# Kernel optimization log

Hardware: AMD Instinct MI355X
Metric: run time of the kernel (lower is better)

## Reference

```python
import jax, jax.numpy as jnp
import numpy as np

N = 50000      # nodes
E = 1600000    # edges (avg degree 32)
D_IN = 128
H = 256        # 2 * out_channels
D_OUT = 128
NEG_SLOPE = 0.2


def setup_inputs() -> dict:
    key = jax.random.key(0)
    ks = jax.random.split(key, 16)
    x = jax.random.normal(ks[0], (N, D_IN), dtype=jnp.float32)
    edge_index = jax.random.randint(ks[1], (2, E), 0, N, dtype=jnp.int64)

    def lin(k, fan_in, fan_out):
        s = 1.0 / np.sqrt(fan_in)
        return jax.random.uniform(k, (fan_in, fan_out), jnp.float32, -s, s)

    def att(k, d):
        s = 1.0 / np.sqrt(d)
        return jax.random.uniform(k, (d,), jnp.float32, -s, s)

    return {
        "x": x, "edge_index": edge_index,
        "W1": lin(ks[2], D_IN, H), "a1_src": att(ks[3], H), "a1_dst": att(ks[4], H), "b1": jnp.zeros((H,), jnp.float32),
        "W2": lin(ks[5], H, H),    "a2_src": att(ks[6], H), "a2_dst": att(ks[7], H), "b2": jnp.zeros((H,), jnp.float32),
        "W3": lin(ks[8], H, D_OUT),"a3_src": att(ks[9], D_OUT), "a3_dst": att(ks[10], D_OUT), "b3": jnp.zeros((D_OUT,), jnp.float32),
    }


def _gat_conv(x, W, a_src, a_dst, b, src, dst):
    # x: [N, Cin] -> h: [N, Cout]
    h = x @ W
    # per-node attention logits, gathered along edges (edge j->i: src=j, dst=i)
    e = jax.nn.leaky_relu((h @ a_src)[src] + (h @ a_dst)[dst], NEG_SLOPE)  # [E]
    # segment softmax over incoming edges of each destination node
    m = jax.ops.segment_max(e, dst, num_segments=N)          # [N]
    p = jnp.exp(e - m[dst])                                  # [E]
    denom = jax.ops.segment_sum(p, dst, num_segments=N)      # [N]
    alpha = p / denom[dst]                                   # [E]
    # scatter-add weighted source features
    out = jax.ops.segment_sum(alpha[:, None] * h[src], dst, num_segments=N)
    return out + b


def reference(x, edge_index, W1, a1_src, a1_dst, b1, W2, a2_src, a2_dst, b2, W3, a3_src, a3_dst, b3):
    src, dst = edge_index[0], edge_index[1]
    h = jax.nn.relu(_gat_conv(x, W1, a1_src, a1_dst, b1, src, dst))
    for _ in range(2):  # hidden_layers, shared conv2 weights
        h = jax.nn.relu(_gat_conv(h, W2, a2_src, a2_dst, b2, src, dst))
    out = _gat_conv(h, W3, a3_src, a3_dst, b3, src, dst)
    return jax.nn.softmax(out, axis=1)
```

## Files before the change

### kernel.cpp

```cpp
#include <hip/hip_runtime.h>
#include <hip/hip_bf16.h>
#include <hip/hip_fp16.h>

#define NN 50000
#define EE 1600000
#define DIN 128
#define HH 256
#define DOUT 128

typedef __attribute__((ext_vector_type(8))) short short8;
typedef __attribute__((ext_vector_type(4))) float f32x4;

__device__ __forceinline__ short f2bf(float v) {
    union { float f; unsigned u; } a;
    a.f = v;
    unsigned r = a.u + 0x7fffu + ((a.u >> 16) & 1u);
    return (short)(r >> 16);
}
__device__ __forceinline__ float bf2f(short h) {
    union { unsigned u; float f; } a;
    a.u = ((unsigned)(unsigned short)h) << 16;
    return a.f;
}


__global__ __launch_bounds__(256) void hist_kernel(const int* __restrict__ dst, int* __restrict__ deg, int E) {
    int e = blockIdx.x * 256 + threadIdx.x;
    if (e < E) atomicAdd(&deg[dst[e]], 1);
}

#define SCAN_B 256

__global__ __launch_bounds__(SCAN_B) void scan1_kernel(const int* __restrict__ deg, int* __restrict__ exc,
                                                       int* __restrict__ bsum, int n) {
    __shared__ int tmp[SCAN_B];
    int i = blockIdx.x * SCAN_B + threadIdx.x;
    int v = (i < n) ? deg[i] : 0;
    tmp[threadIdx.x] = v;
    __syncthreads();
    for (int o = 1; o < SCAN_B; o <<= 1) {
        int t = (threadIdx.x >= o) ? tmp[threadIdx.x - o] : 0;
        __syncthreads();
        tmp[threadIdx.x] += t;
        __syncthreads();
    }
    if (i < n) exc[i] = tmp[threadIdx.x] - v;
    if (threadIdx.x == SCAN_B - 1) bsum[blockIdx.x] = tmp[SCAN_B - 1];
}

__global__ __launch_bounds__(SCAN_B) void scan2_kernel(int* __restrict__ bsum, int nb) {
    __shared__ int tmp[SCAN_B];
    int v = (threadIdx.x < nb) ? bsum[threadIdx.x] : 0;
    tmp[threadIdx.x] = v;
    __syncthreads();
    for (int o = 1; o < SCAN_B; o <<= 1) {
        int t = (threadIdx.x >= o) ? tmp[threadIdx.x - o] : 0;
        __syncthreads();
        tmp[threadIdx.x] += t;
        __syncthreads();
    }
    if (threadIdx.x < nb) bsum[threadIdx.x] = tmp[threadIdx.x] - v;
}

__global__ __launch_bounds__(SCAN_B) void scan3_kernel(int* __restrict__ exc, const int* __restrict__ bsum,
                                                       int* __restrict__ cursor, int n, int E) {
    int i = blockIdx.x * SCAN_B + threadIdx.x;
    if (i < n) {
        int v = exc[i] + bsum[blockIdx.x];
        exc[i] = v;
        cursor[i] = v;
    }
    if (i == n) exc[n] = E;
}

#define NCB 256

__global__ __launch_bounds__(256) void scatter8_kernel(const int* __restrict__ src, const int* __restrict__ dst,
                                                       int* __restrict__ cursor, int* __restrict__ es, int E, int n) {
    int q = blockIdx.x & 7;
    int cb = blockIdx.x >> 3;
    int lo = q * (n >> 3);
    int hi = (q == 7) ? n : lo + (n >> 3);
    int chunk = (E + NCB - 1) / NCB;
    int e1 = min((cb + 1) * chunk, E);
    for (int e = cb * chunk + threadIdx.x; e < e1; e += 256) {
        int d = dst[e];
        if (d >= lo && d < hi) {
            int pos = atomicAdd(&cursor[d], 1);
            es[pos] = src[e];
        }
    }
}


__global__ __launch_bounds__(256) void wsplit_kernel(const float* __restrict__ W, short* __restrict__ WhT,
                                                     short* __restrict__ WlT, int K, int C) {
    int f = blockIdx.x * 256 + threadIdx.x;
    if (f >= K * C) return;
    int k = f / C, c = f % C;
    float v = W[f];
    short h = f2bf(v);
    short l = f2bf(v - bf2f(h));
    WhT[(size_t)c * K + k] = h;
    WlT[(size_t)c * K + k] = l;
}


__global__ __launch_bounds__(256) void tohalf_kernel(const float* __restrict__ in, __half* __restrict__ out,
                                                     size_t cnt) {
    size_t i = (size_t)(blockIdx.x * 256 + threadIdx.x) * 4;
    if (i + 3 < cnt) {
        float4 v = *(const float4*)(in + i);
        __half h0 = __float2half(v.x), h1 = __float2half(v.y);
        __half h2 = __float2half(v.z), h3 = __float2half(v.w);
        __half2* op = (__half2*)(out + i);
        op[0] = __half2(h0, h1);
        op[1] = __half2(h2, h3);
    }
}


template <bool BRELU, bool DOTS, bool HOUT, bool AHIN>
__global__ __launch_bounds__(256) void gemm_mfma_kernel(const float* __restrict__ X, const short* __restrict__ BhT,
                                                        const short* __restrict__ BlT, const float* __restrict__ bias,
                                                        float* __restrict__ out, const float* __restrict__ a1v,
                                                        const float* __restrict__ a2v, float* __restrict__ s1,
                                                        float* __restrict__ s2, int n, int K, int Cout) {
    __shared__ short Ah[128][40], Al[128][40];
    __shared__ short Bh[128][40], Bl[128][40];
    int tid = threadIdx.x;
    int row0 = blockIdx.y * 128, col0 = blockIdx.x * 128;
    int lane = tid & 63, wid = tid >> 6;
    int wr = (wid >> 1) * 64, wc = (wid & 1) * 64;

    f32x4 acc[4][4];
#pragma unroll
    for (int mi = 0; mi < 4; ++mi)
#pragma unroll
        for (int ni = 0; ni < 4; ++ni) acc[mi][ni] = 0.f;

    int srow = tid >> 1;
    int sk = (tid & 1) * 16;

    for (int k0 = 0; k0 < K; k0 += 32) {
        {
            float v[16];
            int gr = row0 + srow;
            if (gr < n) {
                if (AHIN) {
                    const __half* p = (const __half*)X + (size_t)gr * K + k0 + sk;
                    uint4 r0 = ((const uint4*)p)[0];
                    uint4 r1 = ((const uint4*)p)[1];
                    unsigned w[8] = {r0.x, r0.y, r0.z, r0.w, r1.x, r1.y, r1.z, r1.w};
#pragma unroll
                    for (int j = 0; j < 8; ++j) {
                        union { unsigned u; __half2 h; } c;
                        c.u = w[j];
                        float2 f = __half22float2(c.h);
                        v[2 * j] = f.x;
                        v[2 * j + 1] = f.y;
                    }
                } else {
                    const float* p = X + (size_t)gr * K + k0 + sk;
                    float4 f0 = ((const float4*)p)[0];
                    float4 f1 = ((const float4*)p)[1];
                    float4 f2 = ((const float4*)p)[2];
                    float4 f3 = ((const float4*)p)[3];
                    v[0] = f0.x; v[1] = f0.y; v[2] = f0.z; v[3] = f0.w;
                    v[4] = f1.x; v[5] = f1.y; v[6] = f1.z; v[7] = f1.w;
                    v[8] = f2.x; v[9] = f2.y; v[10] = f2.z; v[11] = f2.w;
                    v[12] = f3.x; v[13] = f3.y; v[14] = f3.z; v[15] = f3.w;
                }
            } else {
#pragma unroll
                for (int j = 0; j < 16; ++j) v[j] = 0.f;
            }
            short8 h0, h1, l0, l1;
#pragma unroll
            for (int j = 0; j < 8; ++j) {
                short h = f2bf(v[j]);
                h0[j] = h;
                l0[j] = f2bf(v[j] - bf2f(h));
            }
#pragma unroll
            for (int j = 0; j < 8; ++j) {
                short h = f2bf(v[8 + j]);
                h1[j] = h;
                l1[j] = f2bf(v[8 + j] - bf2f(h));
            }
            *(short8*)&Ah[srow][sk] = h0;
            *(short8*)&Ah[srow][sk + 8] = h1;
            *(short8*)&Al[srow][sk] = l0;
            *(short8*)&Al[srow][sk + 8] = l1;
        }
        {
            const short* ph = BhT + (size_t)(col0 + srow) * K + k0 + sk;
            const short* pl = BlT + (size_t)(col0 + srow) * K + k0 + sk;
            short8 bh0 = ((const short8*)ph)[0];
            short8 bh1 = ((const short8*)ph)[1];
            short8 bl0 = ((const short8*)pl)[0];
            short8 bl1 = ((const short8*)pl)[1];
            *(short8*)&Bh[srow][sk] = bh0;
            *(short8*)&Bh[srow][sk + 8] = bh1;
            *(short8*)&Bl[srow][sk] = bl0;
            *(short8*)&Bl[srow][sk + 8] = bl1;
        }
        __syncthreads();

        int fr = lane & 15, kb = lane >> 4;
        short8 a_h[4], a_l[4];
#pragma unroll
        for (int mi = 0; mi < 4; ++mi) {
            a_h[mi] = *(const short8*)&Ah[wr + mi * 16 + fr][kb * 8];
            a_l[mi] = *(const short8*)&Al[wr + mi * 16 + fr][kb * 8];
        }
#pragma unroll
        for (int ni = 0; ni < 4; ++ni) {
            short8 b_h = *(const short8*)&Bh[wc + ni * 16 + fr][kb * 8];
            short8 b_l = *(const short8*)&Bl[wc + ni * 16 + fr][kb * 8];
#pragma unroll
            for (int mi = 0; mi < 4; ++mi) {
                acc[mi][ni] = __builtin_amdgcn_mfma_f32_16x16x32_bf16(a_l[mi], b_h, acc[mi][ni], 0, 0, 0);
                acc[mi][ni] = __builtin_amdgcn_mfma_f32_16x16x32_bf16(a_h[mi], b_l, acc[mi][ni], 0, 0, 0);
                acc[mi][ni] = __builtin_amdgcn_mfma_f32_16x16x32_bf16(a_h[mi], b_h, acc[mi][ni], 0, 0, 0);
            }
        }
        __syncthreads();
    }

    int dc = lane & 15, dr = (lane >> 4) * 4;

    if (DOTS) {
#pragma unroll
        for (int mi = 0; mi < 4; ++mi) {
#pragma unroll
            for (int r = 0; r < 4; ++r) {
                float p1 = 0.f, p2 = 0.f;
#pragma unroll
                for (int ni = 0; ni < 4; ++ni) {
                    int gcol = col0 + wc + ni * 16 + dc;
                    float v = acc[mi][ni][r];
                    p1 = fmaf(v, a1v[gcol], p1);
                    p2 = fmaf(v, a2v[gcol], p2);
                }
#pragma unroll
                for (int o = 8; o; o >>= 1) {
                    p1 += __shfl_xor(p1, o, 64);
                    p2 += __shfl_xor(p2, o, 64);
                }
                int grow = row0 + wr + mi * 16 + dr + r;
                if (dc == 0 && grow < n) {
                    atomicAdd(s1 + grow, p1);
                    atomicAdd(s2 + grow, p2);
                }
            }
        }
    }

#pragma unroll
    for (int mi = 0; mi < 4; ++mi) {
#pragma unroll
        for (int r = 0; r < 4; ++r) {
            int grow = row0 + wr + mi * 16 + dr + r;
            if (grow >= n) continue;
#pragma unroll
            for (int ni = 0; ni < 4; ++ni) {
                int gcol = col0 + wc + ni * 16 + dc;
                float v = acc[mi][ni][r];
                if (BRELU) {
                    v += bias[gcol];
                    v = fmaxf(v, 0.f);
                }
                if (HOUT) {
                    ((__half*)out)[(size_t)grow * Cout + gcol] = __float2half(v);
                } else {
                    out[(size_t)grow * Cout + gcol] = v;
                }
            }
        }
    }
}


__global__ __launch_bounds__(256) void rowdots_kernel(const float* __restrict__ H, const float* __restrict__ a1,
                                                      const float* __restrict__ a2, float* __restrict__ s1,
                                                      float* __restrict__ s2, int n, int C) {
    int w = (blockIdx.x * 256 + threadIdx.x) >> 6;
    int lane = threadIdx.x & 63;
    if (w >= n) return;
    const float* hp = H + (size_t)w * C;
    float acc1 = 0.f, acc2 = 0.f;
    for (int c = lane; c < C; c += 64) {
        float hv = hp[c];
        acc1 = fmaf(hv, a1[c], acc1);
        acc2 = fmaf(hv, a2[c], acc2);
    }
#pragma unroll
    for (int o = 32; o; o >>= 1) {
        acc1 += __shfl_xor(acc1, o, 64);
        acc2 += __shfl_xor(acc2, o, 64);
    }
    if (lane == 0) {
        s1[w] = acc1;
        s2[w] = acc2;
    }
}


template <int C, bool RELU, bool SOFTMAX, bool OUTH>
__global__ __launch_bounds__(256) void aggf_kernel(const __half* __restrict__ H, const float* __restrict__ ssrc,
                                                   const float* __restrict__ sdst, const int* __restrict__ off,
                                                   const int* __restrict__ es, const float* __restrict__ bias,
                                                   float* __restrict__ out, int n) {
    constexpr int VPL = C / 64;
    int wid = threadIdx.x >> 6, lane = threadIdx.x & 63;
    int node = blockIdx.x * 4 + wid;
    if (node >= n) return;
    int beg = off[node], end = off[node + 1];
    float sd = sdst[node];

    float m = -3e38f;
    for (int e = beg + lane; e < end; e += 64) {
        float g = ssrc[es[e]] + sd;
        g = (g > 0.f) ? g : 0.2f * g;
        m = fmaxf(m, g);
    }
#pragma unroll
    for (int o = 32; o; o >>= 1) m = fmaxf(m, __shfl_xor(m, o, 64));

    float acc[VPL];
#pragma unroll
    for (int v = 0; v < VPL; ++v) acc[v] = 0.f;
    float den = 0.f;
    int c0 = lane * VPL;

    for (int base = beg; base < end; base += 64) {
        int e = base + lane;
        float p = 0.f;
        int s = 0;
        if (e < end) {
            s = es[e];
            float g = ssrc[s] + sd;
            g = (g > 0.f) ? g : 0.2f * g;
            p = __expf(g - m);
            den += p;
        }
        int cnt = end - base;
        if (cnt > 64) cnt = 64;
        int j0 = 0;
        for (; j0 + 8 <= cnt; j0 += 8) {
            float pj[8];
            const __half* hp[8];
#pragma unroll
            for (int u = 0; u < 8; ++u) {
                pj[u] = __shfl(p, j0 + u, 64);
                int sj = __shfl(s, j0 + u, 64);
                hp[u] = H + (size_t)sj * C + c0;
            }
            if (VPL == 4) {
                uint2 raw[8];
#pragma unroll
                for (int u = 0; u < 8; ++u) raw[u] = *(const uint2*)hp[u];
#pragma unroll
                for (int u = 0; u < 8; ++u) {
                    union { unsigned u32; __half2 h2; } lo, hi;
                    lo.u32 = raw[u].x;
                    hi.u32 = raw[u].y;
                    float2 f0 = __half22float2(lo.h2);
                    float2 f1 = __half22float2(hi.h2);
                    acc[0] = fmaf(pj[u], f0.x, acc[0]);
                    acc[1] = fmaf(pj[u], f0.y, acc[1]);
                    acc[2] = fmaf(pj[u], f1.x, acc[2]);
                    acc[3] = fmaf(pj[u], f1.y, acc[3]);
                }
            } else {
                __half2 hv[8];
#pragma unroll
                for (int u = 0; u < 8; ++u) hv[u] = *(const __half2*)hp[u];
#pragma unroll
                for (int u = 0; u < 8; ++u) {
                    float2 f = __half22float2(hv[u]);
                    acc[0] = fmaf(pj[u], f.x, acc[0]);
                    acc[1] = fmaf(pj[u], f.y, acc[1]);
                }
            }
        }
        for (; j0 < cnt; ++j0) {
            float pj = __shfl(p, j0, 64);
            int sj = __shfl(s, j0, 64);
            const __half* hp = H + (size_t)sj * C + c0;
            if (VPL == 4) {
                uint2 raw = *(const uint2*)hp;
                union { unsigned u32; __half2 h2; } lo, hi;
                lo.u32 = raw.x;
                hi.u32 = raw.y;
                float2 f0 = __half22float2(lo.h2);
                float2 f1 = __half22float2(hi.h2);
                acc[0] = fmaf(pj, f0.x, acc[0]);
                acc[1] = fmaf(pj, f0.y, acc[1]);
                acc[2] = fmaf(pj, f1.x, acc[2]);
                acc[3] = fmaf(pj, f1.y, acc[3]);
            } else {
                float2 f = __half22float2(*(const __half2*)hp);
                acc[0] = fmaf(pj, f.x, acc[0]);
                acc[1] = fmaf(pj, f.y, acc[1]);
            }
        }
    }

#pragma unroll
    for (int o = 32; o; o >>= 1) den += __shfl_xor(den, o, 64);
    float inv = (den > 0.f) ? 1.f / den : 0.f;

    float ov[VPL];
#pragma unroll
    for (int v = 0; v < VPL; ++v) {
        float bb = bias ? bias[c0 + v] : 0.f;
        ov[v] = fmaf(acc[v], inv, bb);
        if (RELU) ov[v] = fmaxf(ov[v], 0.f);
    }
    if (SOFTMAX) {
        float mm = ov[0];
#pragma unroll
        for (int v = 1; v < VPL; ++v) mm = fmaxf(mm, ov[v]);
#pragma unroll
        for (int o = 32; o; o >>= 1) mm = fmaxf(mm, __shfl_xor(mm, o, 64));
        float ss = 0.f;
#pragma unroll
        for (int v = 0; v < VPL; ++v) {
            ov[v] = __expf(ov[v] - mm);
            ss += ov[v];
        }
#pragma unroll
        for (int o = 32; o; o >>= 1) ss += __shfl_xor(ss, o, 64);
        float si = 1.f / ss;
#pragma unroll
        for (int v = 0; v < VPL; ++v) ov[v] *= si;
    }
    if (OUTH) {
        __half* op = (__half*)out + (size_t)node * C + c0;
        if (VPL == 4) {
            union { __half2 h2; unsigned u; } w0, w1;
            w0.h2 = __half2(__float2half(ov[0]), __float2half(ov[1]));
            w1.h2 = __half2(__float2half(ov[2]), __float2half(ov[3]));
            uint2 pk;
            pk.x = w0.u;
            pk.y = w1.u;
            *(uint2*)op = pk;
        } else {
            *(__half2*)op = __half2(__float2half(ov[0]), __float2half(ov[1]));
        }
    } else {
        float* op = out + (size_t)node * C + c0;
        if (VPL == 4)
            *(float4*)op = make_float4(ov[0], ov[1], ov[2], ov[3]);
        else
            *(float2*)op = make_float2(ov[0], ov[1]);
    }
}


extern "C" void kernel_launch(void* const* d_in, const int* in_sizes, int n_in,
                              void* d_out, int out_size, void* d_ws, size_t ws_size,
                              hipStream_t stream) {
    const float* x = (const float*)d_in[0];
    const int* ei = (const int*)d_in[1];
    const float* W1 = (const float*)d_in[2];
    const float* a1s = (const float*)d_in[3];
    const float* a1d = (const float*)d_in[4];
    const float* b1 = (const float*)d_in[5];
    const float* W2 = (const float*)d_in[6];
    const float* a2s = (const float*)d_in[7];
    const float* a2d = (const float*)d_in[8];
    const float* b2 = (const float*)d_in[9];
    const float* W3 = (const float*)d_in[10];
    const float* a3s = (const float*)d_in[11];
    const float* a3d = (const float*)d_in[12];
    const float* b3 = (const float*)d_in[13];

    const int n = NN, E = EE;
    const int* src = ei;
    const int* dst = ei + E;

    char* base = (char*)d_ws;
    size_t o = 0;
    auto alloc = [&](size_t bytes) -> char* {
        char* p = base + o;
        o += (bytes + 255) & ~(size_t)255;
        return p;
    };
    int* off = (int*)alloc((n + 1) * sizeof(int));
    int* cur = (int*)alloc((n + 1) * sizeof(int));
    int* bsum = (int*)alloc(1024 * sizeof(int));
    int* es = (int*)alloc((size_t)E * sizeof(int));
    float* sbuf = (float*)alloc((size_t)2 * n * sizeof(float));
    float* ssrc = sbuf;
    float* sdst = sbuf + n;
    float* was = (float*)alloc(256 * sizeof(float));
    float* wad = (float*)alloc(256 * sizeof(float));
    short* W1h = (short*)alloc((size_t)DIN * HH * sizeof(short));
    short* W1l = (short*)alloc((size_t)DIN * HH * sizeof(short));
    short* W2h = (short*)alloc((size_t)HH * HH * sizeof(short));
    short* W2l = (short*)alloc((size_t)HH * HH * sizeof(short));
    short* W3h = (short*)alloc((size_t)HH * DOUT * sizeof(short));
    short* W3l = (short*)alloc((size_t)HH * DOUT * sizeof(short));
    __half* xh = (__half*)alloc((size_t)n * DIN * sizeof(__half));
    __half* Hh = (__half*)alloc((size_t)n * HH * sizeof(__half));
    __half* Abuf = (__half*)alloc((size_t)n * HH * sizeof(__half));
    float* Hbuf = (float*)alloc((size_t)n * DIN * sizeof(float));
    (void)ws_size;

    hipMemsetAsync(cur, 0, (n + 1) * sizeof(int), stream);
    hist_kernel<<<(E + 255) / 256, 256, 0, stream>>>(dst, cur, E);
    int nb = (n + SCAN_B - 1) / SCAN_B;
    scan1_kernel<<<nb, SCAN_B, 0, stream>>>(cur, off, bsum, n);
    scan2_kernel<<<1, SCAN_B, 0, stream>>>(bsum, nb);
    scan3_kernel<<<nb, SCAN_B, 0, stream>>>(off, bsum, cur, n, E);
    scatter8_kernel<<<NCB * 8, 256, 0, stream>>>(src, dst, cur, es, E, n);

    wsplit_kernel<<<(DIN * HH + 255) / 256, 256, 0, stream>>>(W1, W1h, W1l, DIN, HH);
    wsplit_kernel<<<(HH * HH + 255) / 256, 256, 0, stream>>>(W2, W2h, W2l, HH, HH);
    wsplit_kernel<<<(HH * DOUT + 255) / 256, 256, 0, stream>>>(W3, W3h, W3l, HH, DOUT);
    tohalf_kernel<<<((n * DIN / 4) + 255) / 256, 256, 0, stream>>>(x, xh, (size_t)n * DIN);

    int wgrid = (n * 64 + 255) / 256;
    int agrid = (n + 3) / 4;
    int rb = (n + 127) / 128;

    {
        rowdots_kernel<<<(128 * 64 + 255) / 256, 256, 0, stream>>>(W1, a1s, a1d, was, wad, DIN, HH);
        rowdots_kernel<<<wgrid, 256, 0, stream>>>(x, was, wad, ssrc, sdst, n, DIN);
        aggf_kernel<DIN, false, false, false><<<agrid, 256, 0, stream>>>(xh, ssrc, sdst, off, es, nullptr, Hbuf, n);
        dim3 g(HH / 128, rb);
        gemm_mfma_kernel<true, false, true, false><<<g, 256, 0, stream>>>(Hbuf, W1h, W1l, b1, (float*)Abuf, nullptr,
                                                                          nullptr, nullptr, nullptr, n, DIN, HH);
    }
    for (int t = 0; t < 2; ++t) {
        dim3 g(HH / 128, rb);
        hipMemsetAsync(sbuf, 0, (size_t)2 * n * sizeof(float), stream);
        gemm_mfma_kernel<false, true, true, true><<<g, 256, 0, stream>>>((const float*)Abuf, W2h, W2l, nullptr,
                                                                         (float*)Hh, a2s, a2d, ssrc, sdst, n, HH, HH);
        aggf_kernel<HH, true, false, true><<<agrid, 256, 0, stream>>>(Hh, ssrc, sdst, off, es, b2, (float*)Abuf, n);
    }
    {
        dim3 g(DOUT / 128, rb);
        hipMemsetAsync(sbuf, 0, (size_t)2 * n * sizeof(float), stream);
        gemm_mfma_kernel<false, true, true, true><<<g, 256, 0, stream>>>((const float*)Abuf, W3h, W3l, nullptr,
                                                                         (float*)Hh, a3s, a3d, ssrc, sdst, n, HH,
                                                                         DOUT);
        aggf_kernel<DOUT, false, true, false><<<agrid, 256, 0, stream>>>(Hh, ssrc, sdst, off, es, b3, (float*)d_out,
                                                                         n);
    }
}
```

Baseline: 654.7 us.

## Split hidden-layer aggregation into softmax precompute and column-sliced gather kernels

For the two hidden GAT layers, the fused aggregation kernel is replaced by two kernels. The first computes the per-edge exp weights and inverse denominators once and stores packed (src, p) pairs. The second launches one grid pass per 32-column slice, so each wave gathers only 64 bytes per source row, which aims to keep the working set of H in cache and improve locality. The cost is an extra E-sized buffer write and read, plus re-reading the edge lists once per column slice (8 times).

```diff
diff --git a/kernel.cpp b/kernel.cpp
--- a/kernel.cpp
+++ b/kernel.cpp
@@ -303,6 +303,122 @@
     if (lane == 0) {
         s1[w] = acc1;
         s2[w] = acc2;
+    }
+}
+
+
+__global__ __launch_bounds__(256) void mdenp_kernel(const float* __restrict__ ssrc, const float* __restrict__ sdst,
+                                                    const int* __restrict__ off, const int* __restrict__ es,
+                                                    uint2* __restrict__ pae, float* __restrict__ invden, int n) {
+    int w = (blockIdx.x * 256 + threadIdx.x) >> 6;
+    int lane = threadIdx.x & 63;
+    if (w >= n) return;
+    int beg = off[w], end = off[w + 1];
+    float sd = sdst[w];
+    float m = -3e38f;
+    for (int e = beg + lane; e < end; e += 64) {
+        float g = ssrc[es[e]] + sd;
+        g = (g > 0.f) ? g : 0.2f * g;
+        m = fmaxf(m, g);
+    }
+#pragma unroll
+    for (int o = 32; o; o >>= 1) m = fmaxf(m, __shfl_xor(m, o, 64));
+    float den = 0.f;
+    for (int e = beg + lane; e < end; e += 64) {
+        int s = es[e];
+        float g = ssrc[s] + sd;
+        g = (g > 0.f) ? g : 0.2f * g;
+        float p = __expf(g - m);
+        den += p;
+        pae[e] = make_uint2((unsigned)s, __float_as_uint(p));
+    }
+#pragma unroll
+    for (int o = 32; o; o >>= 1) den += __shfl_xor(den, o, 64);
+    if (lane == 0) invden[w] = (den > 0.f) ? 1.f / den : 0.f;
+}
+
+
+template <int C, bool RELU, bool OUTH>
+__global__ __launch_bounds__(256) void aggs_kernel(const __half* __restrict__ H, const uint2* __restrict__ pae,
+                                                   const float* __restrict__ invden, const int* __restrict__ off,
+                                                   const float* __restrict__ bias, void* __restrict__ out, int n,
+                                                   int chunks) {
+    int pass = blockIdx.x / chunks;
+    int chunk = blockIdx.x % chunks;
+    int wid = threadIdx.x >> 6, lane = threadIdx.x & 63;
+    int node = chunk * 4 + wid;
+    if (node >= n) return;
+    int beg = off[node], end = off[node + 1];
+    int g = lane >> 4, cl = lane & 15;
+    int col = pass * 32 + cl * 2;
+    const __half2* Hc = (const __half2*)(H + col);
+
+    float a0 = 0.f, a1 = 0.f;
+    for (int base = beg; base < end; base += 64) {
+        int e = base + lane;
+        float al = 0.f;
+        int s = 0;
+        if (e < end) {
+            uint2 r = pae[e];
+            s = (int)r.x;
+            al = __uint_as_float(r.y);
+        }
+        int cnt = end - base;
+        if (cnt > 64) cnt = 64;
+        int j0 = 0;
+        for (; j0 + 16 <= cnt; j0 += 16) {
+            float pj[4];
+            const __half2* hp[4];
+#pragma unroll
+            for (int u = 0; u < 4; ++u) {
+                int j = j0 + u * 4 + g;
+                pj[u] = __shfl(al, j, 64);
+                int sj = __shfl(s, j, 64);
+                hp[u] = Hc + (size_t)sj * (C / 2);
+            }
+            __half2 hv[4];
+#pragma unroll
+            for (int u = 0; u < 4; ++u) hv[u] = *hp[u];
+#pragma unroll
+            for (int u = 0; u < 4; ++u) {
+                float2 f = __half22float2(hv[u]);
+                a0 = fmaf(pj[u], f.x, a0);
+                a1 = fmaf(pj[u], f.y, a1);
+            }
+        }
+        for (; j0 < cnt; j0 += 4) {
+            int j = j0 + g;
+            bool ok = j < cnt;
+            int jj = ok ? j : cnt - 1;
+            float pj = __shfl(al, jj, 64);
+            if (!ok) pj = 0.f;
+            int sj = __shfl(s, jj, 64);
+            float2 f = __half22float2(Hc[(size_t)sj * (C / 2)]);
+            a0 = fmaf(pj, f.x, a0);
+            a1 = fmaf(pj, f.y, a1);
+        }
+    }
+
+    a0 += __shfl_xor(a0, 16, 64);
+    a1 += __shfl_xor(a1, 16, 64);
+    a0 += __shfl_xor(a0, 32, 64);
+    a1 += __shfl_xor(a1, 32, 64);
+
+    if (g == 0) {
+        float inv = invden[node];
+        float b0 = bias ? bias[col] : 0.f;
+        float b1 = bias ? bias[col + 1] : 0.f;
+        float o0 = fmaf(a0, inv, b0);
+        float o1 = fmaf(a1, inv, b1);
+        if (RELU) {
+            o0 = fmaxf(o0, 0.f);
+            o1 = fmaxf(o1, 0.f);
+        }
+        if (OUTH) {
+            *((__half2*)((__half*)out + (size_t)node * C + col)) = __half2(__float2half(o0), __float2half(o1));
+        } else {
+            *((float2*)((float*)out + (size_t)node * C + col)) = make_float2(o0, o1);
+        }
     }
 }
 
@@ -493,9 +609,11 @@
     int* cur = (int*)alloc((n + 1) * sizeof(int));
     int* bsum = (int*)alloc(1024 * sizeof(int));
     int* es = (int*)alloc((size_t)E * sizeof(int));
+    uint2* pae = (uint2*)alloc((size_t)E * sizeof(uint2));
     float* sbuf = (float*)alloc((size_t)2 * n * sizeof(float));
     float* ssrc = sbuf;
     float* sdst = sbuf + n;
+    float* invden = (float*)alloc((size_t)n * sizeof(float));
     float* was = (float*)alloc(256 * sizeof(float));
     float* wad = (float*)alloc(256 * sizeof(float));
     short* W1h = (short*)alloc((size_t)DIN * HH * sizeof(short));
@@ -540,7 +658,9 @@
         hipMemsetAsync(sbuf, 0, (size_t)2 * n * sizeof(float), stream);
         gemm_mfma_kernel<false, true, true, true><<<g, 256, 0, stream>>>((const float*)Abuf, W2h, W2l, nullptr,
                                                                          (float*)Hh, a2s, a2d, ssrc, sdst, n, HH, HH);
-        aggf_kernel<HH, true, false, true><<<agrid, 256, 0, stream>>>(Hh, ssrc, sdst, off, es, b2, (float*)Abuf, n);
+        mdenp_kernel<<<wgrid, 256, 0, stream>>>(ssrc, sdst, off, es, pae, invden, n);
+        aggs_kernel<HH, true, true><<<(HH / 32) * agrid, 256, 0, stream>>>(Hh, pae, invden, off, b2, (void*)Abuf, n,
+                                                                           agrid);
     }
     {
         dim3 g(DOUT / 128, rb);
```

New measurement: 837.4 us. +27.9%, slower.

## Replace per-node softmax max pass with global source-score upper bound

Applied to the files above, without the earlier changes.

Drops the first edge pass in the aggregation kernel, which computed the exact per-destination max of the attention logits. It instead uses leaky_relu(global max of ssrc + sdst[node]) as the stabilizing constant, found by a small grid-wide atomicMax reduction before each aggregation. Softmax is invariant to the shift, so this is mathematically valid. The catch is that if a node's logits sit far below the bound, exp can underflow. The first layer's aggregate is also now written in half precision instead of float, halving that intermediate's traffic into the GEMM.

```diff
diff --git a/kernel.cpp b/kernel.cpp
--- a/kernel.cpp
+++ b/kernel.cpp
@@ -117,6 +117,28 @@
         op[0] = __half2(h0, h1);
         op[1] = __half2(h2, h3);
     }
+}
+
+
+__global__ __launch_bounds__(256) void gmax_kernel(const float* __restrict__ s, unsigned* __restrict__ gm, int n) {
+    int i0 = blockIdx.x * 256 + threadIdx.x;
+    float m = -3e38f;
+    for (int i = i0; i < n; i += 256 * 64) m = fmaxf(m, s[i]);
+#pragma unroll
+    for (int o = 32; o; o >>= 1) m = fmaxf(m, __shfl_xor(m, o, 64));
+    if ((threadIdx.x & 63) == 0) {
+        union { float f; unsigned u; } a;
+        a.f = m;
+        unsigned v = (a.u & 0x80000000u) ? ~a.u : (a.u | 0x80000000u);
+        atomicMax(gm, v);
+    }
+}
+
+__device__ __forceinline__ float unmap_max(unsigned v) {
+    unsigned u = (v & 0x80000000u) ? (v ^ 0x80000000u) : ~v;
+    union { unsigned u; float f; } a;
+    a.u = u;
+    return a.f;
 }
 
 
@@ -311,22 +333,15 @@
 __global__ __launch_bounds__(256) void aggf_kernel(const __half* __restrict__ H, const float* __restrict__ ssrc,
                                                    const float* __restrict__ sdst, const int* __restrict__ off,
                                                    const int* __restrict__ es, const float* __restrict__ bias,
-                                                   float* __restrict__ out, int n) {
+                                                   float* __restrict__ out, const unsigned* __restrict__ gmu, int n) {
     constexpr int VPL = C / 64;
     int wid = threadIdx.x >> 6, lane = threadIdx.x & 63;
     int node = blockIdx.x * 4 + wid;
     if (node >= n) return;
     int beg = off[node], end = off[node + 1];
     float sd = sdst[node];
-
-    float m = -3e38f;
-    for (int e = beg + lane; e < end; e += 64) {
-        float g = ssrc[es[e]] + sd;
-        g = (g > 0.f) ? g : 0.2f * g;
-        m = fmaxf(m, g);
-    }
-#pragma unroll
-    for (int o = 32; o; o >>= 1) m = fmaxf(m, __shfl_xor(m, o, 64));
+    float m = unmap_max(gmu[0]) + sd;
+    m = (m > 0.f) ? m : 0.2f * m;
 
     float acc[VPL];
 #pragma unroll
@@ -496,6 +511,7 @@
     float* sbuf = (float*)alloc((size_t)2 * n * sizeof(float));
     float* ssrc = sbuf;
     float* sdst = sbuf + n;
+    unsigned* gmu = (unsigned*)alloc(256);
     float* was = (float*)alloc(256 * sizeof(float));
     float* wad = (float*)alloc(256 * sizeof(float));
     short* W1h = (short*)alloc((size_t)DIN * HH * sizeof(short));
@@ -505,9 +521,9 @@
     short* W3h = (short*)alloc((size_t)HH * DOUT * sizeof(short));
     short* W3l = (short*)alloc((size_t)HH * DOUT * sizeof(short));
     __half* xh = (__half*)alloc((size_t)n * DIN * sizeof(__half));
+    __half* Zh = (__half*)alloc((size_t)n * DIN * sizeof(__half));
     __half* Hh = (__half*)alloc((size_t)n * HH * sizeof(__half));
     __half* Abuf = (__half*)alloc((size_t)n * HH * sizeof(__half));
-    float* Hbuf = (float*)alloc((size_t)n * DIN * sizeof(float));
     (void)ws_size;
 
     hipMemsetAsync(cur, 0, (n + 1) * sizeof(int), stream);
@@ -530,25 +546,34 @@
     {
         rowdots_kernel<<<(128 * 64 + 255) / 256, 256, 0, stream>>>(W1, a1s, a1d, was, wad, DIN, HH);
         rowdots_kernel<<<wgrid, 256, 0, stream>>>(x, was, wad, ssrc, sdst, n, DIN);
-        aggf_kernel<DIN, false, false, false><<<agrid, 256, 0, stream>>>(xh, ssrc, sdst, off, es, nullptr, Hbuf, n);
+        hipMemsetAsync(gmu, 0, 4, stream);
+        gmax_kernel<<<64, 256, 0, stream>>>(ssrc, gmu, n);
+        aggf_kernel<DIN, false, false, true><<<agrid, 256, 0, stream>>>(xh, ssrc, sdst, off, es, nullptr, (float*)Zh,
+                                                                        gmu, n);
         dim3 g(HH / 128, rb);
-        gemm_mfma_kernel<true, false, true, false><<<g, 256, 0, stream>>>(Hbuf, W1h, W1l, b1, (float*)Abuf, nullptr,
-                                                                          nullptr, nullptr, nullptr, n, DIN, HH);
+        gemm_mfma_kernel<true, false, true, true><<<g, 256, 0, stream>>>((const float*)Zh, W1h, W1l, b1,
+                                                                         (float*)Abuf, nullptr, nullptr, nullptr,
+                                                                         nullptr, n, DIN, HH);
     }
     for (int t = 0; t < 2; ++t) {
         dim3 g(HH / 128, rb);
         hipMemsetAsync(sbuf, 0, (size_t)2 * n * sizeof(float), stream);
+        hipMemsetAsync(gmu, 0, 4, stream);
         gemm_mfma_kernel<false, true, true, true><<<g, 256, 0, stream>>>((const float*)Abuf, W2h, W2l, nullptr,
                                                                          (float*)Hh, a2s, a2d, ssrc, sdst, n, HH, HH);
-        aggf_kernel<HH, true, false, true><<<agrid, 256, 0, stream>>>(Hh, ssrc, sdst, off, es, b2, (float*)Abuf, n);
+        gmax_kernel<<<64, 256, 0, stream>>>(ssrc, gmu, n);
+        aggf_kernel<HH, true, false, true><<<agrid, 256, 0, stream>>>(Hh, ssrc, sdst, off, es, b2, (float*)Abuf, gmu,
+                                                                      n);
     }
     {
         dim3 g(DOUT / 128, rb);
         hipMemsetAsync(sbuf, 0, (size_t)2 * n * sizeof(float), stream);
+        hipMemsetAsync(gmu, 0, 4, stream);
         gemm_mfma_kernel<false, true, true, true><<<g, 256, 0, stream>>>((const float*)Abuf, W3h, W3l, nullptr,
                                                                          (float*)Hh, a3s, a3d, ssrc, sdst, n, HH,
                                                                          DOUT);
+        gmax_kernel<<<64, 256, 0, stream>>>(ssrc, gmu, n);
         aggf_kernel<DOUT, false, true, false><<<agrid, 256, 0, stream>>>(Hh, ssrc, sdst, off, es, b3, (float*)d_out,
-                                                                         n);
-    }
-}
+                                                                         gmu, n);
+    }
+}
```

Result: no change. 666.3 us (+1.8%).
